# Kernel tuning notes

Measured on AMD Instinct MI355X. Metric: run time of the kernel, lower is better.

The kernel has to match this reference:

```python
import jax, jax.numpy as jnp
import numpy as np

D_MODEL = 512
NUM_HEADS = 8
HEAD_DIM = D_MODEL // NUM_HEADS
BATCH = 4
SEQ = 2048
ROPE_BASE = 10000.0


def rope_cos_sin(seq_len, head_dim):
    inv_freq = 1.0 / (ROPE_BASE ** (jnp.arange(0, head_dim, 2, dtype=jnp.float32) / head_dim))
    t = jnp.arange(seq_len, dtype=jnp.float32)
    freqs = jnp.outer(t, inv_freq)              # (S, head_dim/2)
    emb = jnp.concatenate([freqs, freqs], axis=-1)  # (S, head_dim)
    return jnp.cos(emb), jnp.sin(emb)


def apply_rope(x, cos, sin):
    # x: (..., S, head_dim); cos/sin: (S, head_dim)
    x1 = x[..., ::2]
    x2 = x[..., 1::2]
    ch = cos[..., ::2]
    sh = sin[..., ::2]
    r1 = x1 * ch - x2 * sh
    r2 = x1 * sh + x2 * ch
    return jnp.stack([r1, r2], axis=-1).reshape(x.shape)


def setup_inputs() -> dict:
    key = jax.random.key(0)
    ks = jax.random.split(key, 12)
    x = jax.random.normal(ks[0], (BATCH, SEQ, D_MODEL), dtype=jnp.float32)
    variate_ids = jnp.sort(jax.random.randint(ks[1], (BATCH, SEQ), 0, 8), axis=-1).astype(jnp.int64)
    mask = jnp.ones((BATCH, SEQ), dtype=jnp.float32)
    s = 1.0 / np.sqrt(D_MODEL)
    Wq = jax.random.normal(ks[2], (D_MODEL, D_MODEL), dtype=jnp.float32) * s
    bq = jnp.zeros((D_MODEL,), dtype=jnp.float32)
    Wk = jax.random.normal(ks[3], (D_MODEL, D_MODEL), dtype=jnp.float32) * s
    bk = jnp.zeros((D_MODEL,), dtype=jnp.float32)
    Wv = jax.random.normal(ks[4], (D_MODEL, D_MODEL), dtype=jnp.float32) * s
    bv = jnp.zeros((D_MODEL,), dtype=jnp.float32)
    Wo = jax.random.normal(ks[5], (D_MODEL, D_MODEL), dtype=jnp.float32) * s
    bo = jnp.zeros((D_MODEL,), dtype=jnp.float32)
    u_same = jax.random.normal(ks[6], (NUM_HEADS,), dtype=jnp.float32) * 0.1
    u_cross = jax.random.normal(ks[7], (NUM_HEADS,), dtype=jnp.float32) * 0.1
    return dict(x=x, variate_ids=variate_ids, mask=mask, Wq=Wq, bq=bq, Wk=Wk, bk=bk,
                Wv=Wv, bv=bv, Wo=Wo, bo=bo, u_same=u_same, u_cross=u_cross)


def reference(x, variate_ids, mask, Wq, bq, Wk, bk, Wv, bv, Wo, bo, u_same, u_cross):
    B, S, D = x.shape
    H, Hd = NUM_HEADS, HEAD_DIM
    scale = 1.0 / np.sqrt(Hd)

    def proj(W, b):
        return (x @ W.T + b).reshape(B, S, H, Hd).transpose(0, 2, 1, 3)  # (B,H,S,Hd)

    q = proj(Wq, bq)
    k = proj(Wk, bk)
    v = proj(Wv, bv)

    cos, sin = rope_cos_sin(S, Hd)
    q = apply_rope(q, cos, sin)
    k = apply_rope(k, cos, sin)

    scores = jnp.einsum('bhid,bhjd->bhij', q, k) * scale  # (B,H,S,S)
    same = (variate_ids[:, :, None] == variate_ids[:, None, :]).astype(jnp.float32)  # (B,S,S)
    bias = same[:, None] * u_same[None, :, None, None] + (1.0 - same)[:, None] * u_cross[None, :, None, None]
    scores = scores + bias
    scores = scores + (1.0 - mask[:, None, None, :]) * -1e9
    probs = jax.nn.softmax(scores, axis=-1)
    out = jnp.einsum('bhij,bhjd->bhid', probs, v)  # (B,H,S,Hd)
    out = out.transpose(0, 2, 1, 3).reshape(B, S, D)
    return out @ Wo.T + bo
```

## Files before the change

### kernel.cpp

```cpp
#include <hip/hip_runtime.h>
#include <hip/hip_bf16.h>

#define BATCH   4
#define SEQ     2048
#define DMODEL  512
#define NHEADS  8
#define HEADDIM 64
#define MTOT    (BATCH*SEQ)
#define NX      (MTOT*DMODEL)
#define NW      (DMODEL*DMODEL)
#define QTILE   64
#define KTILE   32
#define NKT_G   32

#define LOG2E   1.4426950408889634f
#define SCL2    0.18033688011112042f
#define SHIFT   14.426950408889634f
#define BIGL    1.4426950408889634e9f

typedef unsigned short u16;
typedef __bf16 bf16x8 __attribute__((ext_vector_type(8)));
typedef float  f32x4  __attribute__((ext_vector_type(4)));
typedef unsigned short u16x4 __attribute__((ext_vector_type(4)));
typedef unsigned u32x2 __attribute__((ext_vector_type(2)));

#define MFMA(a,b,c) __builtin_amdgcn_mfma_f32_16x16x32_bf16(a,b,c,0,0,0)

__device__ __forceinline__ u16 f2bf(float f) {
    unsigned u = __float_as_uint(f);
    u += 0x7FFFu + ((u >> 16) & 1u);
    return (u16)(u >> 16);
}
__device__ __forceinline__ unsigned pk_bf16(float a, float b) {
    union { __hip_bfloat162 h; unsigned u; } cv;
    cv.h = __float22bfloat162_rn(make_float2(a, b));
    return cv.u;
}
__device__ __forceinline__ void gll16(const void* g, void* l) {
    __builtin_amdgcn_global_load_lds((const __attribute__((address_space(1))) void*)g,
                                     (__attribute__((address_space(3))) void*)l, 16, 0, 0);
}
__device__ __forceinline__ void gll4(const void* g, void* l) {
    __builtin_amdgcn_global_load_lds((const __attribute__((address_space(1))) void*)g,
                                     (__attribute__((address_space(3))) void*)l, 4, 0, 0);
}

#define NCVT4 ((NX + 4*NW)/4)
__global__ __launch_bounds__(256) void cvt_rope_kernel(
    const float* __restrict__ x,
    const float* __restrict__ wq, const float* __restrict__ wk,
    const float* __restrict__ wv, const float* __restrict__ wo,
    u16* __restrict__ xbf,
    u16* __restrict__ wqbf, u16* __restrict__ wkbf,
    u16* __restrict__ wvbf, u16* __restrict__ wobf,
    float2* __restrict__ cst)
{
    int i4 = blockIdx.x * 256 + threadIdx.x;
    if (i4 < NCVT4) {
        int i = i4 * 4;
        const float* s; u16* d; int o;
        if (i < NX) { s = x; d = xbf; o = i; }
        else {
            int j = i - NX;
            int r = j >> 18;
            o = j & (NW - 1);
            s = (r == 0) ? wq : (r == 1) ? wk : (r == 2) ? wv : wo;
            d = (r == 0) ? wqbf : (r == 1) ? wkbf : (r == 2) ? wvbf : wobf;
        }
        float4 v = *(const float4*)(s + o);
        u16x4 u = { f2bf(v.x), f2bf(v.y), f2bf(v.z), f2bf(v.w) };
        *(u16x4*)(d + o) = u;
    } else {
        int r = i4 - NCVT4;
        if (r < SEQ * 32 / 4) {
            int idx = r * 4;
            int s  = idx >> 5;
            int p0 = idx & 31;
#pragma unroll
            for (int t = 0; t < 4; ++t) {
                int p = p0 + t;
                float inv = __expf(-0.5756462732485115f * (float)(p & 15));
                float ang = (float)s * inv;
                cst[idx + t] = make_float2(cosf(ang), sinf(ang));
            }
        }
    }
}

#define TP 136
__global__ __launch_bounds__(256) void qkv_kernel(
    const u16* __restrict__ x,
    const u16* __restrict__ Wq, const float* __restrict__ bq,
    const u16* __restrict__ Wk, const float* __restrict__ bk,
    const u16* __restrict__ Wv, const float* __restrict__ bv,
    const float* __restrict__ cstf,
    u16* __restrict__ qws, u16* __restrict__ kws, u16* __restrict__ vtws)
{
    __shared__ alignas(16) u16 smem[128 * TP];
    u16* As = smem;
    u16* Bs = smem + 8192;

    const int m0 = blockIdx.x * 128;
    const int n0 = blockIdx.y * 128;
    const int tid  = threadIdx.x;
    const int w    = tid >> 6;
    const int lane = tid & 63;
    const int quad = lane >> 4;
    const int l16  = lane & 15;
    const int wm = w & 1, wn = w >> 1;

    const int sec = n0 >> 9;
    const int oc0 = n0 & 511;
    const u16*   Wm = (sec == 0) ? Wq : (sec == 1 ? Wk : Wv);
    const float* bb = (sec == 0) ? bq : (sec == 1 ? bk : bv);

    const int xb = (sec < 2) ? wn : wm;
    const int wb = (sec < 2) ? wm : wn;

    f32x4 acc[4][4] = {};

    for (int kb = 0; kb < 8; ++kb) {
#pragma unroll
        for (int it = 0; it < 4; ++it) {
            const int s   = it * 256 + tid;
            const int row = s >> 3;
            const int cb  = s & 7;
            const int gcol = kb * 64 + (((cb ^ (row & 7))) << 3);
            gll16(x  + (m0  + row) * 512 + gcol, &As[s * 8]);
            gll16(Wm + (oc0 + row) * 512 + gcol, &Bs[s * 8]);
        }
        __syncthreads();

#pragma unroll
        for (int ks = 0; ks < 2; ++ks) {
            bf16x8 xf[4], wf[4];
#pragma unroll
            for (int t = 0; t < 4; ++t) {
                const int xrow = xb * 64 + t * 16 + l16;
                const int wrow = wb * 64 + t * 16 + l16;
                xf[t] = *(const bf16x8*)&As[xrow * 64 + (((ks * 4 + quad) ^ (xrow & 7)) << 3)];
                wf[t] = *(const bf16x8*)&Bs[wrow * 64 + (((ks * 4 + quad) ^ (wrow & 7)) << 3)];
            }
            if (sec < 2) {
#pragma unroll
                for (int tm = 0; tm < 4; ++tm)
#pragma unroll
                    for (int tn = 0; tn < 4; ++tn)
                        acc[tm][tn] = MFMA(wf[tm], xf[tn], acc[tm][tn]);
            } else {
#pragma unroll
                for (int tm = 0; tm < 4; ++tm)
#pragma unroll
                    for (int tn = 0; tn < 4; ++tn)
                        acc[tm][tn] = MFMA(xf[tm], wf[tn], acc[tm][tn]);
            }
        }
        __syncthreads();
    }

    if (sec < 2) {
#pragma unroll
        for (int tm = 0; tm < 4; ++tm) {
            const int dls = wm * 64 + tm * 16 + quad * 4;
            const float4 bv4 = *(const float4*)&bb[oc0 + dls];
            const int pbase = ((oc0 + dls) & 63) >> 1;
#pragma unroll
            for (int tn = 0; tn < 4; ++tn) {
                const int sl = wn * 64 + tn * 16 + l16;
                const int sg = (m0 + sl) & 2047;
                const float4 cs = *(const float4*)&cstf[sg * 64 + pbase * 2];
                const float v0 = acc[tm][tn][0] + bv4.x;
                const float v1 = acc[tm][tn][1] + bv4.y;
                const float v2 = acc[tm][tn][2] + bv4.z;
                const float v3 = acc[tm][tn][3] + bv4.w;
                const float r0 = v0 * cs.x - v1 * cs.y;
                const float r1 = v1 * cs.x + v0 * cs.y;
                const float r2 = v2 * cs.z - v3 * cs.w;
                const float r3 = v3 * cs.z + v2 * cs.w;
                u32x2 pv = { pk_bf16(r0, r1), pk_bf16(r2, r3) };
                *(u32x2*)&smem[sl * TP + dls] = pv;
            }
        }
        __syncthreads();
        u16* dst0 = (sec == 0) ? qws : kws;
#pragma unroll
        for (int i = 0; i < 8; ++i) {
            const int c   = i * 256 + tid;
            const int sl  = c >> 4;
            const int d8  = (c & 15) * 8;
            const int gcol = oc0 + d8;
            const int hh  = gcol >> 6;
            const int dh  = gcol & 63;
            const int sgl = m0 + sl;
            const int bi  = sgl >> 11;
            const int s   = sgl & 2047;
            u16* dst = dst0 + (size_t)(bi * NHEADS + hh) * (SEQ * HEADDIM)
                            + (size_t)s * HEADDIM + dh;
            *(bf16x8*)dst = *(const bf16x8*)&smem[sl * TP + d8];
        }
    } else {
#pragma unroll
        for (int tm = 0; tm < 4; ++tm) {
            const int row_l = wm * 64 + tm * 16 + quad * 4;
#pragma unroll
            for (int tn = 0; tn < 4; ++tn) {
                const int col_l = wn * 64 + tn * 16 + l16;
                const float bval = bb[oc0 + col_l];
                u32x2 pv = { pk_bf16(acc[tm][tn][0] + bval, acc[tm][tn][1] + bval),
                             pk_bf16(acc[tm][tn][2] + bval, acc[tm][tn][3] + bval) };
                *(u32x2*)&smem[col_l * TP + row_l] = pv;
            }
        }
        __syncthreads();
        const int bi  = m0 >> 11;
        const int sgb = m0 & 2047;
#pragma unroll
        for (int i = 0; i < 8; ++i) {
            const int c    = i * 256 + tid;
            const int col  = c >> 4;
            const int sc8  = (c & 15) * 8;
            const int gcol = oc0 + col;
            const int hh   = gcol >> 6;
            const int d    = gcol & 63;
            u16* dst = vtws + (size_t)(bi * NHEADS + hh) * (SEQ * HEADDIM)
                            + (size_t)d * SEQ + sgb + sc8;
            *(bf16x8*)dst = *(const bf16x8*)&smem[col * TP + sc8];
        }
    }
}

__global__ __launch_bounds__(512, 6) void attn_kernel(
    const u16* __restrict__ qws, const u16* __restrict__ kws,
    const u16* __restrict__ vtl,
    const int* __restrict__ vids, const float* __restrict__ mask,
    const float* __restrict__ u_same, const float* __restrict__ u_cross,
    u16* __restrict__ attn)
{
    __shared__ alignas(16) u16 smem[16384];
    __shared__ alignas(16) u16 plsm[8 * 16 * 40];
    __shared__ int   bidm[2][2][KTILE];
    __shared__ float bmkm[2][2][KTILE];
    __shared__ float comb_li2[2][QTILE];

    const int id  = blockIdx.y * 32 + blockIdx.x;
    const int xcd = id & 7;
    const int idx = id >> 3;
    const int bh  = xcd * 4 + (idx & 3);
    const int q0  = (idx >> 2) * QTILE;
    const int b   = bh >> 3;
    const int h   = bh & 7;

    const int tid  = threadIdx.x;
    const int w    = tid >> 6;
    const int lane = tid & 63;
    const int quad = lane >> 4;
    const int l16  = lane & 15;
    const int qw   = w & 3;
    const int kg   = w >> 2;
    const int tl   = tid & 255;

    const float us2 = u_same[h]  * LOG2E;
    const float uc2 = u_cross[h] * LOG2E;
    const float uc3 = uc2 - BIGL - SHIFT;
    const float du2 = us2 - uc2;
    const size_t tb = (size_t)bh * (SEQ * HEADDIM);

    const int qr = q0 + qw * 16 + l16;
    const bf16x8 aq0 = *(const bf16x8*)(qws + tb + qr * HEADDIM + quad * 8);
    const bf16x8 aq1 = *(const bf16x8*)(qws + tb + qr * HEADDIM + 32 + quad * 8);

    const int vq = vids[b * SEQ + q0 + qw * 16 + l16];

    float li = 0.f;
    f32x4 o[4] = {};

    const int srow  = tl >> 3;
    const int scb   = tl & 7;
    const int soff  = ((scb ^ (srow & 7)) << 3);
    const int vrow  = tl >> 2;
    const int vcb   = (tl & 3) ^ ((vrow >> 1) & 3);
    const int soffv = (vcb << 3);
    const int kbase = kg * 2 * 2048;

    auto stage = [&](int t, int nb) {
        const int k0 = (kg * NKT_G + t) * KTILE;
        gll16(kws + tb + (size_t)(k0 + srow) * HEADDIM + soff,
              &smem[kbase + nb * 2048 + tl * 8]);
        gll16(vtl + tb + (size_t)vrow * SEQ + k0 + soffv,
              &smem[8192 + kbase + nb * 2048 + tl * 8]);
        if (tl < KTILE) {
            gll4(vids + b * SEQ + k0 + tl, &bidm[kg][nb][0]);
            gll4(mask + b * SEQ + k0 + tl, &bmkm[kg][nb][0]);
        }
    };

    u16* const pw = &plsm[w * 640];

    auto body = [&](const int cur) {
        const u16* kb_b = &smem[kbase + cur * 2048];
        const u16* vb_b = &smem[8192 + kbase + cur * 2048];
#pragma unroll
        for (int nt = 0; nt < 2; ++nt) {
            const int krow = nt * 16 + l16;
            const int r7   = krow & 7;
            const bf16x8 kb0 = *(const bf16x8*)&kb_b[krow * 64 + ((quad ^ r7) << 3)];
            const bf16x8 kb1 = *(const bf16x8*)&kb_b[krow * 64 + ((quad ^ r7 ^ 4) << 3)];
            f32x4 sc = {};
            sc = MFMA(kb0, aq0, sc);
            sc = MFMA(kb1, aq1, sc);
            const int kk = nt * 16 + quad * 4;
            const int4   kv4 = *(const int4*)&bidm[kg][cur][kk];
            const float4 mk4 = *(const float4*)&bmkm[kg][cur][kk];
            const int   kvr[4] = { kv4.x, kv4.y, kv4.z, kv4.w };
            const float mkr[4] = { mk4.x, mk4.y, mk4.z, mk4.w };
            float p[4];
#pragma unroll
            for (int r = 0; r < 4; ++r) {
                const float sel = fmaf(mkr[r], BIGL, uc3) + ((kvr[r] == vq) ? du2 : 0.0f);
                p[r] = __builtin_amdgcn_exp2f(fmaf(sc[r], SCL2, sel));
                li += p[r];
            }
            u32x2 pv = { pk_bf16(p[0], p[1]), pk_bf16(p[2], p[3]) };
            *(u32x2*)&pw[l16 * 40 + nt * 16 + quad * 4] = pv;
        }

        const bf16x8 ap = *(const bf16x8*)&pw[l16 * 40 + quad * 8];

#pragma unroll
        for (int nt = 0; nt < 4; ++nt) {
            const int vr = nt * 16 + l16;
            const bf16x8 vb0 = *(const bf16x8*)&vb_b[vr * 32 + (((quad ^ ((vr >> 1) & 3))) << 3)];
            o[nt] = MFMA(ap, vb0, o[nt]);
        }
    };

    stage(0, 0);
    for (int t = 0; t < NKT_G; t += 2) {
        __syncthreads();
        stage(t + 1, 1);
        body(0);
        __syncthreads();
        if (t + 2 < NKT_G) stage(t + 2, 0);
        body(1);
    }

    float liq = li + __shfl_xor(li, 16);
    liq += __shfl_xor(liq, 32);
    __syncthreads();
    float* co = (float*)smem;
    if (quad == 0) comb_li2[kg][qw * 16 + l16] = liq;
    if (kg == 1) {
#pragma unroll
        for (int nt = 0; nt < 4; ++nt)
#pragma unroll
            for (int r = 0; r < 4; ++r)
                co[(qw * 16 + quad * 4 + r) * 65 + nt * 16 + l16] = o[nt][r];
    }
    __syncthreads();
    if (kg == 0) {
#pragma unroll
        for (int r = 0; r < 4; ++r) {
            const int qloc = qw * 16 + quad * 4 + r;
            const float lt = comb_li2[0][qloc] + comb_li2[1][qloc];
            const float inv = 1.0f / lt;
            const int R  = q0 + qloc;
            const int rb = (b * SEQ + R) * DMODEL + h * HEADDIM;
#pragma unroll
            for (int nt = 0; nt < 4; ++nt)
                attn[rb + nt * 16 + l16] =
                    f2bf((o[nt][r] + co[qloc * 65 + nt * 16 + l16]) * inv);
        }
    }
}

__global__ __launch_bounds__(256) void proj_kernel(
    const u16* __restrict__ a, const u16* __restrict__ Wo,
    const float* __restrict__ bo, float* __restrict__ out)
{
    __shared__ alignas(16) u16 psm[132 * 64 * 2];
    u16* As = psm;
    u16* Bs = psm + 8192;
    float* Lp = (float*)psm;

    const int m0 = blockIdx.x * 128;
    const int n0 = blockIdx.y * 128;
    const int tid  = threadIdx.x;
    const int w    = tid >> 6;
    const int lane = tid & 63;
    const int quad = lane >> 4;
    const int l16  = lane & 15;
    const int wm = w & 1, wn = w >> 1;

    f32x4 acc[4][4] = {};

    for (int kb = 0; kb < 8; ++kb) {
#pragma unroll
        for (int it = 0; it < 4; ++it) {
            const int s   = it * 256 + tid;
            const int row = s >> 3;
            const int cb  = s & 7;
            const int gcol = kb * 64 + (((cb ^ (row & 7))) << 3);
            gll16(a  + (m0 + row) * 512 + gcol, &As[s * 8]);
            gll16(Wo + (n0 + row) * 512 + gcol, &Bs[s * 8]);
        }
        __syncthreads();

#pragma unroll
        for (int ks = 0; ks < 2; ++ks) {
            bf16x8 af[4], wf[4];
#pragma unroll
            for (int t = 0; t < 4; ++t) {
                const int arow = wn * 64 + t * 16 + l16;
                const int wrow = wm * 64 + t * 16 + l16;
                af[t] = *(const bf16x8*)&As[arow * 64 + (((ks * 4 + quad) ^ (arow & 7)) << 3)];
                wf[t] = *(const bf16x8*)&Bs[wrow * 64 + (((ks * 4 + quad) ^ (wrow & 7)) << 3)];
            }
#pragma unroll
            for (int tm = 0; tm < 4; ++tm)
#pragma unroll
                for (int tn = 0; tn < 4; ++tn)
                    acc[tm][tn] = MFMA(wf[tm], af[tn], acc[tm][tn]);
        }
        __syncthreads();
    }

#pragma unroll
    for (int hph = 0; hph < 2; ++hph) {
        if (wn == hph) {
#pragma unroll
            for (int tm = 0; tm < 4; ++tm) {
                const int dls = wm * 64 + tm * 16 + quad * 4;
                const float4 bv4 = *(const float4*)&bo[n0 + dls];
#pragma unroll
                for (int tn = 0; tn < 4; ++tn) {
                    const int s2 = tn * 16 + l16;
                    float4 v = { acc[tm][tn][0] + bv4.x, acc[tm][tn][1] + bv4.y,
                                 acc[tm][tn][2] + bv4.z, acc[tm][tn][3] + bv4.w };
                    *(float4*)&Lp[s2 * 132 + dls] = v;
                }
            }
        }
        __syncthreads();
#pragma unroll
        for (int i = 0; i < 8; ++i) {
            const int c  = i * 256 + tid;
            const int s2 = c >> 5;
            const int dq = (c & 31) * 4;
            float4 v = *(const float4*)&Lp[s2 * 132 + dq];
            *(float4*)&out[(size_t)(m0 + hph * 64 + s2) * 512 + n0 + dq] = v;
        }
        __syncthreads();
    }
}

extern "C" void kernel_launch(void* const* d_in, const int* in_sizes, int n_in,
                              void* d_out, int out_size, void* d_ws, size_t ws_size,
                              hipStream_t stream) {
    const float* x    = (const float*)d_in[0];
    const int*   vids = (const int*)d_in[1];
    const float* mask = (const float*)d_in[2];
    const float* Wq = (const float*)d_in[3];
    const float* bq = (const float*)d_in[4];
    const float* Wk = (const float*)d_in[5];
    const float* bk = (const float*)d_in[6];
    const float* Wv = (const float*)d_in[7];
    const float* bv = (const float*)d_in[8];
    const float* Wo = (const float*)d_in[9];
    const float* bo = (const float*)d_in[10];
    const float* usame  = (const float*)d_in[11];
    const float* ucross = (const float*)d_in[12];
    float* out = (float*)d_out;

    u16* xbf  = (u16*)d_ws;
    u16* wqbf = xbf + NX;
    u16* wkbf = wqbf + NW;
    u16* wvbf = wkbf + NW;
    u16* wobf = wvbf + NW;
    float2* cst = (float2*)(wobf + NW);
    u16* qws  = (u16*)(cst + SEQ * 32);
    u16* kws  = qws + (size_t)BATCH * NHEADS * SEQ * HEADDIM;
    u16* vtws = kws + (size_t)BATCH * NHEADS * SEQ * HEADDIM;
    u16* attn = xbf;

    cvt_rope_kernel<<<(NCVT4 + SEQ * 32 / 4 + 255) / 256, 256, 0, stream>>>(
        x, Wq, Wk, Wv, Wo, xbf, wqbf, wkbf, wvbf, wobf, cst);

    dim3 g1(MTOT / 128, 3 * DMODEL / 128);
    qkv_kernel<<<g1, 256, 0, stream>>>(xbf, wqbf, bq, wkbf, bk, wvbf, bv,
                                       (const float*)cst, qws, kws, vtws);

    dim3 g2(SEQ / QTILE, BATCH * NHEADS);
    attn_kernel<<<g2, 512, 0, stream>>>(qws, kws, vtws, vids, mask,
                                        usame, ucross, attn);

    dim3 g3(MTOT / 128, DMODEL / 128);
    proj_kernel<<<g3, 256, 0, stream>>>(attn, wobf, bo, out);
}
```

Measured before the change: 194.0 us.

## Use permlane swaps for P fragment, precompute mask bias, add MFMA priority hints

The attention inner loop no longer routes the softmax probability tile through per-wave LDS. When the compiler exposes the gfx950 permlane32/permlane16 swap builtins, it rearranges the packed bf16 values across lanes in registers. A precomputed additive mask term is also written in the conversion kernel, so the per-element bias in the softmax becomes a single add plus select. s_setprio hints are placed around the MFMA groups to favour matrix issue across waves. The LDS fallback stays for compilers without the builtins.

```diff
diff --git a/kernel.cpp b/kernel.cpp
--- a/kernel.cpp
+++ b/kernel.cpp
@@ -18,6 +18,12 @@
 #define SHIFT   14.426950408889634f
 #define BIGL    1.4426950408889634e9f
 
+#if __has_builtin(__builtin_amdgcn_permlane32_swap) && __has_builtin(__builtin_amdgcn_permlane16_swap)
+#define HAS_PERMLANE 1
+#else
+#define HAS_PERMLANE 0
+#endif
+
 typedef unsigned short u16;
 typedef __bf16 bf16x8 __attribute__((ext_vector_type(8)));
 typedef float  f32x4  __attribute__((ext_vector_type(4)));
@@ -46,14 +52,17 @@
 }
 
 #define NCVT4 ((NX + 4*NW)/4)
+#define NCST4 (SEQ * 32 / 4)
+#define NMSK4 (BATCH * SEQ / 4)
 __global__ __launch_bounds__(256) void cvt_rope_kernel(
     const float* __restrict__ x,
     const float* __restrict__ wq, const float* __restrict__ wk,
     const float* __restrict__ wv, const float* __restrict__ wo,
+    const float* __restrict__ mask,
     u16* __restrict__ xbf,
     u16* __restrict__ wqbf, u16* __restrict__ wkbf,
     u16* __restrict__ wvbf, u16* __restrict__ wobf,
-    float2* __restrict__ cst)
+    float2* __restrict__ cst, float* __restrict__ Mws)
 {
     int i4 = blockIdx.x * 256 + threadIdx.x;
     if (i4 < NCVT4) {
@@ -72,7 +81,7 @@
         *(u16x4*)(d + o) = u;
     } else {
         int r = i4 - NCVT4;
-        if (r < SEQ * 32 / 4) {
+        if (r < NCST4) {
             int idx = r * 4;
             int s  = idx >> 5;
             int p0 = idx & 31;
@@ -83,6 +92,12 @@
                 float ang = (float)s * inv;
                 cst[idx + t] = make_float2(cosf(ang), sinf(ang));
             }
+        } else if (r < NCST4 + NMSK4) {
+            int idx = (r - NCST4) * 4;
+            float4 mv = *(const float4*)&mask[idx];
+            float4 ov = { fmaf(mv.x - 1.0f, BIGL, -SHIFT), fmaf(mv.y - 1.0f, BIGL, -SHIFT),
+                          fmaf(mv.z - 1.0f, BIGL, -SHIFT), fmaf(mv.w - 1.0f, BIGL, -SHIFT) };
+            *(float4*)&Mws[idx] = ov;
         }
     }
 }
@@ -232,12 +247,14 @@
 __global__ __launch_bounds__(512, 6) void attn_kernel(
     const u16* __restrict__ qws, const u16* __restrict__ kws,
     const u16* __restrict__ vtl,
-    const int* __restrict__ vids, const float* __restrict__ mask,
+    const int* __restrict__ vids, const float* __restrict__ Mws,
     const float* __restrict__ u_same, const float* __restrict__ u_cross,
     u16* __restrict__ attn)
 {
     __shared__ alignas(16) u16 smem[16384];
+#if !HAS_PERMLANE
     __shared__ alignas(16) u16 plsm[8 * 16 * 40];
+#endif
     __shared__ int   bidm[2][2][KTILE];
     __shared__ float bmkm[2][2][KTILE];
     __shared__ float comb_li2[2][QTILE];
@@ -261,8 +278,6 @@
 
     const float us2 = u_same[h]  * LOG2E;
     const float uc2 = u_cross[h] * LOG2E;
-    const float uc3 = uc2 - BIGL - SHIFT;
-    const float du2 = us2 - uc2;
     const size_t tb = (size_t)bh * (SEQ * HEADDIM);
 
     const int qr = q0 + qw * 16 + l16;
@@ -290,15 +305,18 @@
               &smem[8192 + kbase + nb * 2048 + tl * 8]);
         if (tl < KTILE) {
             gll4(vids + b * SEQ + k0 + tl, &bidm[kg][nb][0]);
-            gll4(mask + b * SEQ + k0 + tl, &bmkm[kg][nb][0]);
+            gll4(Mws  + b * SEQ + k0 + tl, &bmkm[kg][nb][0]);
         }
     };
 
+#if !HAS_PERMLANE
     u16* const pw = &plsm[w * 640];
+#endif
 
     auto body = [&](const int cur) {
         const u16* kb_b = &smem[kbase + cur * 2048];
         const u16* vb_b = &smem[8192 + kbase + cur * 2048];
+        unsigned x0, x1, y0, y1;
 #pragma unroll
         for (int nt = 0; nt < 2; ++nt) {
             const int krow = nt * 16 + l16;
@@ -306,8 +324,10 @@
             const bf16x8 kb0 = *(const bf16x8*)&kb_b[krow * 64 + ((quad ^ r7) << 3)];
             const bf16x8 kb1 = *(const bf16x8*)&kb_b[krow * 64 + ((quad ^ r7 ^ 4) << 3)];
             f32x4 sc = {};
+            __builtin_amdgcn_s_setprio(1);
             sc = MFMA(kb0, aq0, sc);
             sc = MFMA(kb1, aq1, sc);
+            __builtin_amdgcn_s_setprio(0);
             const int kk = nt * 16 + quad * 4;
             const int4   kv4 = *(const int4*)&bidm[kg][cur][kk];
             const float4 mk4 = *(const float4*)&bmkm[kg][cur][kk];
@@ -316,22 +336,37 @@
             float p[4];
 #pragma unroll
             for (int r = 0; r < 4; ++r) {
-                const float sel = fmaf(mkr[r], BIGL, uc3) + ((kvr[r] == vq) ? du2 : 0.0f);
+                const float sel = mkr[r] + ((kvr[r] == vq) ? us2 : uc2);
                 p[r] = __builtin_amdgcn_exp2f(fmaf(sc[r], SCL2, sel));
                 li += p[r];
             }
-            u32x2 pv = { pk_bf16(p[0], p[1]), pk_bf16(p[2], p[3]) };
-            *(u32x2*)&pw[l16 * 40 + nt * 16 + quad * 4] = pv;
-        }
-
-        const bf16x8 ap = *(const bf16x8*)&pw[l16 * 40 + quad * 8];
-
+            if (nt == 0) { x0 = pk_bf16(p[0], p[1]); x1 = pk_bf16(p[2], p[3]); }
+            else         { y0 = pk_bf16(p[0], p[1]); y1 = pk_bf16(p[2], p[3]); }
+        }
+
+        union { unsigned u[4]; bf16x8 v; } ap;
+#if HAS_PERMLANE
+        auto s0 = __builtin_amdgcn_permlane32_swap(x0, y0, false, false);
+        auto t0 = __builtin_amdgcn_permlane16_swap(s0[0], s0[1], false, false);
+        auto s1 = __builtin_amdgcn_permlane32_swap(x1, y1, false, false);
+        auto t1 = __builtin_amdgcn_permlane16_swap(s1[0], s1[1], false, false);
+        ap.u[0] = t0[0]; ap.u[1] = t1[0]; ap.u[2] = t0[1]; ap.u[3] = t1[1];
+#else
+        u32x2 pv0 = { x0, x1 };
+        u32x2 pv1 = { y0, y1 };
+        *(u32x2*)&pw[l16 * 40 + quad * 4]      = pv0;
+        *(u32x2*)&pw[l16 * 40 + 16 + quad * 4] = pv1;
+        ap.v = *(const bf16x8*)&pw[l16 * 40 + quad * 8];
+#endif
+
+        __builtin_amdgcn_s_setprio(1);
 #pragma unroll
         for (int nt = 0; nt < 4; ++nt) {
             const int vr = nt * 16 + l16;
             const bf16x8 vb0 = *(const bf16x8*)&vb_b[vr * 32 + (((quad ^ ((vr >> 1) & 3))) << 3)];
-            o[nt] = MFMA(ap, vb0, o[nt]);
-        }
+            o[nt] = MFMA(ap.v, vb0, o[nt]);
+        }
+        __builtin_amdgcn_s_setprio(0);
     };
 
     stage(0, 0);
@@ -477,20 +512,21 @@
     u16* wvbf = wkbf + NW;
     u16* wobf = wvbf + NW;
     float2* cst = (float2*)(wobf + NW);
-    u16* qws  = (u16*)(cst + SEQ * 32);
+    float*  Mws = (float*)(cst + SEQ * 32);
+    u16* qws  = (u16*)(Mws + BATCH * SEQ);
     u16* kws  = qws + (size_t)BATCH * NHEADS * SEQ * HEADDIM;
     u16* vtws = kws + (size_t)BATCH * NHEADS * SEQ * HEADDIM;
     u16* attn = xbf;
 
-    cvt_rope_kernel<<<(NCVT4 + SEQ * 32 / 4 + 255) / 256, 256, 0, stream>>>(
-        x, Wq, Wk, Wv, Wo, xbf, wqbf, wkbf, wvbf, wobf, cst);
+    cvt_rope_kernel<<<(NCVT4 + NCST4 + NMSK4 + 255) / 256, 256, 0, stream>>>(
+        x, Wq, Wk, Wv, Wo, mask, xbf, wqbf, wkbf, wvbf, wobf, cst, Mws);
 
     dim3 g1(MTOT / 128, 3 * DMODEL / 128);
     qkv_kernel<<<g1, 256, 0, stream>>>(xbf, wqbf, bq, wkbf, bk, wvbf, bv,
                                        (const float*)cst, qws, kws, vtws);
 
     dim3 g2(SEQ / QTILE, BATCH * NHEADS);
-    attn_kernel<<<g2, 512, 0, stream>>>(qws, kws, vtws, vids, mask,
+    attn_kernel<<<g2, 512, 0, stream>>>(qws, kws, vtws, vids, Mws,
                                         usame, ucross, attn);
 
     dim3 g3(MTOT / 128, DMODEL / 128);
```

Result: no change. 190.4 us (-1.9%).
